# Kernel tuning notes

Measured on AMD Instinct MI355X. Metric: run time of the kernel, lower is better.

The kernel has to match this reference:

```python
import jax, jax.numpy as jnp
import numpy as np

U1, U2 = 128, 32  # GRU units


def gru(x, kernel, rec_kernel, bias, act, rec_act):
    """Keras GRU with reset_after=True. x: [B,T,F], kernel: [F,3U],
    rec_kernel: [U,3U], bias: [2,3U] (input bias, recurrent bias).
    Gate order is [z, r, h]. Returns (sequence [B,T,U], last state [B,U])."""
    B = x.shape[0]
    U = rec_kernel.shape[0]
    # Precompute the input projection for all timesteps in one big matmul.
    xb = jnp.einsum('btf,fg->btg', x, kernel) + bias[0]  # [B,T,3U]

    def step(h, xt):
        inner = h @ rec_kernel + bias[1]                 # [B,3U]
        xz, xr, xh = jnp.split(xt, 3, axis=-1)
        iz, ir, ih = jnp.split(inner, 3, axis=-1)
        z = rec_act(xz + iz)
        r = rec_act(xr + ir)
        hh = act(xh + r * ih)
        h_new = z * h + (1.0 - z) * hh
        return h_new, h_new

    h0 = jnp.zeros((B, U), x.dtype)
    hT, hs = jax.lax.scan(step, h0, jnp.swapaxes(xb, 0, 1))  # scan over T
    return jnp.swapaxes(hs, 0, 1), hT


def setup_inputs() -> dict:
    key = jax.random.key(0)
    ks = jax.random.split(key, 9)
    B, T, F = 512, 1024, 1
    s = 0.05
    return {
        'x':   jax.random.normal(ks[0], (B, T, F), jnp.float32),
        'k1':  jax.random.normal(ks[1], (F, 3 * U1), jnp.float32) * s,
        'rk1': jax.random.normal(ks[2], (U1, 3 * U1), jnp.float32) * s,
        'b1':  jnp.zeros((2, 3 * U1), jnp.float32),
        'k2':  jax.random.normal(ks[3], (U1, 3 * U2), jnp.float32) * s,
        'rk2': jax.random.normal(ks[4], (U2, 3 * U2), jnp.float32) * s,
        'b2':  jnp.zeros((2, 3 * U2), jnp.float32),
        'wd':  jax.random.normal(ks[5], (U2, 1), jnp.float32) * s,
        'bd':  jnp.zeros((1,), jnp.float32),
    }


def reference(x, k1, rk1, b1, k2, rk2, b2, wd, bd):
    # GRU-1: activation=tanh, recurrent_activation=relu, return_sequences=True
    seq1, _ = gru(x, k1, rk1, b1, jnp.tanh, jax.nn.relu)
    # Dropout(0.5) is identity at inference time.
    # GRU-2: activation=relu, recurrent_activation=sigmoid, return last state
    _, h2 = gru(seq1, k2, rk2, b2, jax.nn.relu, jax.nn.sigmoid)
    return h2 @ wd + bd  # [B,1]
```

## Files before the change

kernel.cpp:

```cpp
#include <hip/hip_runtime.h>
#include <math.h>

#define TT 1024
#define U1 128
#define U2 32
#define NCOL 480
#define NCP 240
#define NUQ 4

__device__ __forceinline__ float fast_tanh(float v) {
    float e = __expf(2.f * v);
    return 1.f - 2.f / (e + 1.f);
}
__device__ __forceinline__ float fast_sig(float v) {
    return 1.f / (1.f + __expf(-v));
}

__global__ __launch_bounds__(1024)
void gru_stack_kernel(const float* __restrict__ x,
                      const float* __restrict__ k1,
                      const float* __restrict__ rk1,
                      const float* __restrict__ b1,
                      const float* __restrict__ k2,
                      const float* __restrict__ rk2,
                      const float* __restrict__ b2,
                      const float* __restrict__ wd,
                      const float* __restrict__ bd,
                      float* __restrict__ out)
{
    __shared__ __align__(16) float h1s[2][U1];
    __shared__ __align__(16) float h2s[2][U2];
    __shared__ __align__(16) float part1[2][NUQ][NCOL];
    __shared__ __align__(16) float part2[2][96];

    const int t  = threadIdx.x;
    const int b0 = blockIdx.x * 2;

    if (t < 2 * U1) ((float*)h1s)[t] = 0.f;
    if (t < 2 * U2) ((float*)h2s)[t] = 0.f;

    float2 w2[32];
    const float4* pb0 = nullptr;
    const float4* pb1 = nullptr;
    float2* pd0 = nullptr;
    float2* pd1 = nullptr;
    const bool is_dot = (t < 1008);
    if (t < 960) {
        const int uq = t / NCP, p = t % NCP;
        const int c0 = 2 * p, ub = 32 * uq;
#pragma unroll
        for (int j = 0; j < 32; ++j) {
            const int u = ub + j;
            float vv[2];
#pragma unroll
            for (int r = 0; r < 2; ++r) {
                const int c = c0 + r;
                vv[r] = (c < 384) ? rk1[u * 384 + c] : k2[u * 96 + (c - 384)];
            }
            w2[j] = make_float2(vv[0], vv[1]);
        }
        pb0 = (const float4*)&h1s[0][ub];
        pb1 = (const float4*)&h1s[1][ub];
        pd0 = (float2*)&part1[0][uq][c0];
        pd1 = (float2*)&part1[1][uq][c0];
    } else if (t < 1008) {
        const int q2 = t - 960, c0 = 2 * q2;
#pragma unroll
        for (int j = 0; j < 32; ++j)
            w2[j] = make_float2(rk2[j * 96 + c0 + 0], rk2[j * 96 + c0 + 1]);
        pb0 = (const float4*)&h2s[0][0];
        pb1 = (const float4*)&h2s[1][0];
        pd0 = (float2*)&part2[0][c0];
        pd1 = (float2*)&part2[1][c0];
    }

    const int ju = t & 127, bu = t >> 7;
    float k1z = 0, k1r = 0, k1h = 0, bz = 0, br = 0, bhx = 0, bhr = 0, h_old = 0;
    if (t < 256) {
        k1z = k1[ju]; k1r = k1[128 + ju]; k1h = k1[256 + ju];
        bz  = b1[ju]       + b1[384 + ju];
        br  = b1[128 + ju] + b1[384 + 128 + ju];
        bhx = b1[256 + ju];
        bhr = b1[384 + 256 + ju];
    }
    const int tau = t - 256, j2 = tau & 31, bb2 = tau >> 5;
    float bz2 = 0, br2 = 0, bh2x = 0, bh2r = 0, h2_old = 0;
    if (t >= 256 && t < 320) {
        bz2  = b2[j2]      + b2[96 + j2];
        br2  = b2[32 + j2] + b2[96 + 32 + j2];
        bh2x = b2[64 + j2];
        bh2r = b2[96 + 64 + j2];
    }

    __syncthreads();

    for (int i = 0; i <= TT; ++i) {
        float xv = 0.f;
        if (t < 256 && i < TT) xv = x[(b0 + bu) * TT + i];

        if (is_dot) {
            float2 a0 = make_float2(0.f, 0.f);
            float2 a1 = make_float2(0.f, 0.f);
#pragma unroll
            for (int j4 = 0; j4 < 8; ++j4) {
                float4 hv0 = pb0[j4];
                float4 hv1 = pb1[j4];
                float ha0[4] = {hv0.x, hv0.y, hv0.z, hv0.w};
                float ha1[4] = {hv1.x, hv1.y, hv1.z, hv1.w};
#pragma unroll
                for (int e = 0; e < 4; ++e) {
                    const float2 wv = w2[4 * j4 + e];
                    const float he0 = ha0[e], he1 = ha1[e];
                    a0.x = fmaf(he0, wv.x, a0.x);
                    a0.y = fmaf(he0, wv.y, a0.y);
                    a1.x = fmaf(he1, wv.x, a1.x);
                    a1.y = fmaf(he1, wv.y, a1.y);
                }
            }
            *pd0 = a0;
            *pd1 = a1;
        }
        __syncthreads();

        if (t < 256 && i < TT) {
            float iz = part1[bu][0][ju] + part1[bu][1][ju]
                     + part1[bu][2][ju] + part1[bu][3][ju];
            float ir = part1[bu][0][128 + ju] + part1[bu][1][128 + ju]
                     + part1[bu][2][128 + ju] + part1[bu][3][128 + ju];
            float ih = part1[bu][0][256 + ju] + part1[bu][1][256 + ju]
                     + part1[bu][2][256 + ju] + part1[bu][3][256 + ju];
            float z  = fmaxf(fmaf(xv, k1z, bz) + iz, 0.f);
            float r  = fmaxf(fmaf(xv, k1r, br) + ir, 0.f);
            float hh = fast_tanh(fmaf(xv, k1h, bhx) + r * (ih + bhr));
            h_old = fmaf(z, h_old - hh, hh);
            h1s[bu][ju] = h_old;
        } else if (t >= 256 && t < 320 && i >= 1) {
            float xz = part1[bb2][0][384 + j2] + part1[bb2][1][384 + j2]
                     + part1[bb2][2][384 + j2] + part1[bb2][3][384 + j2];
            float xr = part1[bb2][0][416 + j2] + part1[bb2][1][416 + j2]
                     + part1[bb2][2][416 + j2] + part1[bb2][3][416 + j2];
            float xh = part1[bb2][0][448 + j2] + part1[bb2][1][448 + j2]
                     + part1[bb2][2][448 + j2] + part1[bb2][3][448 + j2];
            float iz = part2[bb2][j2];
            float ir = part2[bb2][32 + j2];
            float ih = part2[bb2][64 + j2];
            float z  = fast_sig(xz + iz + bz2);
            float r  = fast_sig(xr + ir + br2);
            float hh = fmaxf(xh + bh2x + r * (ih + bh2r), 0.f);
            h2_old = fmaf(z, h2_old - hh, hh);
            h2s[bb2][j2] = h2_old;
        }
        __syncthreads();
    }

    if (t < 64) {
        const int b = t >> 5, j = t & 31;
        float p = h2s[b][j] * wd[j];
#pragma unroll
        for (int m = 16; m >= 1; m >>= 1) p += __shfl_xor(p, m, 64);
        if (j == 0) out[b0 + b] = p + bd[0];
    }
}

extern "C" void kernel_launch(void* const* d_in, const int* in_sizes, int n_in,
                              void* d_out, int out_size, void* d_ws, size_t ws_size,
                              hipStream_t stream) {
    const float* x   = (const float*)d_in[0];
    const float* k1  = (const float*)d_in[1];
    const float* rk1 = (const float*)d_in[2];
    const float* b1  = (const float*)d_in[3];
    const float* k2  = (const float*)d_in[4];
    const float* rk2 = (const float*)d_in[5];
    const float* b2  = (const float*)d_in[6];
    const float* wd  = (const float*)d_in[7];
    const float* bd  = (const float*)d_in[8];
    float* out = (float*)d_out;

    dim3 grid(256), block(1024);
    hipLaunchKernelGGL(gru_stack_kernel, grid, block, 0, stream,
                       x, k1, rk1, b1, k2, rk2, b2, wd, bd, out);
}
```

Measured before the change: 1.143 ms.

## Transpose partial-sum shared layout for float4 reads and stage x in LDS

Stores the per-quarter partial dot products transposed, so each gate consumer fetches its four partials with one 128-bit LDS read instead of four scalar reads. Layer-2 recurrent partials get the same treatment. The whole input sequence for the block's two batch rows is preloaded into shared memory, which removes a global load from every timestep. The cost is scattered scalar stores on the producer side, with possible bank conflicts, and extra shared memory use.

```diff
diff --git a/kernel.cpp b/kernel.cpp
--- a/kernel.cpp
+++ b/kernel.cpp
@@ -15,6 +15,9 @@
 __device__ __forceinline__ float fast_sig(float v) {
     return 1.f / (1.f + __expf(-v));
 }
+__device__ __forceinline__ float hsum4(float4 v) {
+    return (v.x + v.y) + (v.z + v.w);
+}
 
 __global__ __launch_bounds__(1024)
 void gru_stack_kernel(const float* __restrict__ x,
@@ -30,20 +33,24 @@
 {
     __shared__ __align__(16) float h1s[2][U1];
     __shared__ __align__(16) float h2s[2][U2];
-    __shared__ __align__(16) float part1[2][NUQ][NCOL];
-    __shared__ __align__(16) float part2[2][96];
+    __shared__ __align__(16) float part1T[2][NCOL][4];
+    __shared__ __align__(16) float part2T[2][U2][4];
+    __shared__ __align__(16) float xs[2][TT];
 
     const int t  = threadIdx.x;
     const int b0 = blockIdx.x * 2;
 
     if (t < 2 * U1) ((float*)h1s)[t] = 0.f;
     if (t < 2 * U2) ((float*)h2s)[t] = 0.f;
+    for (int idx = t; idx < 2 * TT; idx += 1024)
+        ((float*)xs)[idx] = x[b0 * TT + idx];
 
     float2 w2[32];
     const float4* pb0 = nullptr;
     const float4* pb1 = nullptr;
-    float2* pd0 = nullptr;
-    float2* pd1 = nullptr;
+    float* pd0 = nullptr;
+    float* pd1 = nullptr;
+    int pstride = 4;
     const bool is_dot = (t < 1008);
     if (t < 960) {
         const int uq = t / NCP, p = t % NCP;
@@ -61,8 +68,9 @@
         }
         pb0 = (const float4*)&h1s[0][ub];
         pb1 = (const float4*)&h1s[1][ub];
-        pd0 = (float2*)&part1[0][uq][c0];
-        pd1 = (float2*)&part1[1][uq][c0];
+        pd0 = &part1T[0][c0][uq];
+        pd1 = &part1T[1][c0][uq];
+        pstride = 4;
     } else if (t < 1008) {
         const int q2 = t - 960, c0 = 2 * q2;
 #pragma unroll
@@ -70,8 +78,9 @@
             w2[j] = make_float2(rk2[j * 96 + c0 + 0], rk2[j * 96 + c0 + 1]);
         pb0 = (const float4*)&h2s[0][0];
         pb1 = (const float4*)&h2s[1][0];
-        pd0 = (float2*)&part2[0][c0];
-        pd1 = (float2*)&part2[1][c0];
+        pd0 = &part2T[0][c0 & 31][c0 >> 5];
+        pd1 = &part2T[1][c0 & 31][c0 >> 5];
+        pstride = (((c0 + 1) & 31) - (c0 & 31)) * 4 + (((c0 + 1) >> 5) - (c0 >> 5));
     }
 
     const int ju = t & 127, bu = t >> 7;
@@ -95,9 +104,6 @@
     __syncthreads();
 
     for (int i = 0; i <= TT; ++i) {
-        float xv = 0.f;
-        if (t < 256 && i < TT) xv = x[(b0 + bu) * TT + i];
-
         if (is_dot) {
             float2 a0 = make_float2(0.f, 0.f);
             float2 a1 = make_float2(0.f, 0.f);
@@ -117,36 +123,35 @@
                     a1.y = fmaf(he1, wv.y, a1.y);
                 }
             }
-            *pd0 = a0;
-            *pd1 = a1;
+            pd0[0] = a0.x; pd0[pstride] = a0.y;
+            pd1[0] = a1.x; pd1[pstride] = a1.y;
         }
         __syncthreads();
 
         if (t < 256 && i < TT) {
-            float iz = part1[bu][0][ju] + part1[bu][1][ju]
-                     + part1[bu][2][ju] + part1[bu][3][ju];
-            float ir = part1[bu][0][128 + ju] + part1[bu][1][128 + ju]
-                     + part1[bu][2][128 + ju] + part1[bu][3][128 + ju];
-            float ih = part1[bu][0][256 + ju] + part1[bu][1][256 + ju]
-                     + part1[bu][2][256 + ju] + part1[bu][3][256 + ju];
+            const float xv = xs[bu][i];
+            const float4 iz4 = *(const float4*)&part1T[bu][ju][0];
+            const float4 ir4 = *(const float4*)&part1T[bu][128 + ju][0];
+            const float4 ih4 = *(const float4*)&part1T[bu][256 + ju][0];
+            float iz = hsum4(iz4);
+            float ir = hsum4(ir4);
+            float ih = hsum4(ih4);
             float z  = fmaxf(fmaf(xv, k1z, bz) + iz, 0.f);
             float r  = fmaxf(fmaf(xv, k1r, br) + ir, 0.f);
             float hh = fast_tanh(fmaf(xv, k1h, bhx) + r * (ih + bhr));
             h_old = fmaf(z, h_old - hh, hh);
             h1s[bu][ju] = h_old;
         } else if (t >= 256 && t < 320 && i >= 1) {
-            float xz = part1[bb2][0][384 + j2] + part1[bb2][1][384 + j2]
-                     + part1[bb2][2][384 + j2] + part1[bb2][3][384 + j2];
-            float xr = part1[bb2][0][416 + j2] + part1[bb2][1][416 + j2]
-                     + part1[bb2][2][416 + j2] + part1[bb2][3][416 + j2];
-            float xh = part1[bb2][0][448 + j2] + part1[bb2][1][448 + j2]
-                     + part1[bb2][2][448 + j2] + part1[bb2][3][448 + j2];
-            float iz = part2[bb2][j2];
-            float ir = part2[bb2][32 + j2];
-            float ih = part2[bb2][64 + j2];
-            float z  = fast_sig(xz + iz + bz2);
-            float r  = fast_sig(xr + ir + br2);
-            float hh = fmaxf(xh + bh2x + r * (ih + bh2r), 0.f);
+            const float4 xz4 = *(const float4*)&part1T[bb2][384 + j2][0];
+            const float4 xr4 = *(const float4*)&part1T[bb2][416 + j2][0];
+            const float4 xh4 = *(const float4*)&part1T[bb2][448 + j2][0];
+            const float4 in4 = *(const float4*)&part2T[bb2][j2][0];
+            float xz = hsum4(xz4);
+            float xr = hsum4(xr4);
+            float xh = hsum4(xh4);
+            float z  = fast_sig(xz + in4.x + bz2);
+            float r  = fast_sig(xr + in4.y + br2);
+            float hh = fmaxf(xh + bh2x + r * (in4.z + bh2r), 0.f);
             h2_old = fmaf(z, h2_old - hh, hh);
             h2s[bb2][j2] = h2_old;
         }
```

Result: slower. 1.411 ms (+23.5%).
